# Kernel tuning notes

Measured on AMD Instinct MI355X. Metric: run time of the kernel, lower is better.

Reference implementation:

```python
import jax, jax.numpy as jnp
import numpy as np

N = 100000      # num nodes
E = 600000      # num edges
DIN = 64        # input_dim
DH = 128        # hidden_dim
G = 512         # num graphs
EPS = 1e-5      # BatchNorm eps


def setup_inputs() -> dict:
    key = jax.random.key(0)
    ks = jax.random.split(key, 12)
    x = jax.random.normal(ks[0], (N, DIN), jnp.float32)
    edge_index = jax.random.randint(ks[1], (2, E), 0, N)
    batch = jnp.sort(jax.random.randint(ks[2], (N,), 0, G))

    def w(k, shape):
        return (jax.random.normal(k, shape, jnp.float32) / np.float32(np.sqrt(shape[0])))

    inp = {"x": x, "edge_index": edge_index, "batch": batch}
    inp.update(
        W1=w(ks[3], (DIN, DH)), b1=jnp.zeros((DH,), jnp.float32),
        bn1_g=jnp.ones((DH,), jnp.float32), bn1_b=jnp.zeros((DH,), jnp.float32),
        bn1_m=jax.random.normal(ks[4], (DH,), jnp.float32) * 0.1,
        bn1_v=jnp.ones((DH,), jnp.float32),
        W2=w(ks[5], (DH, DH)), b2=jnp.zeros((DH,), jnp.float32),
        bn2_g=jnp.ones((DH,), jnp.float32), bn2_b=jnp.zeros((DH,), jnp.float32),
        bn2_m=jax.random.normal(ks[6], (DH,), jnp.float32) * 0.1,
        bn2_v=jnp.ones((DH,), jnp.float32),
        W3=w(ks[7], (DH, DH)), b3=jnp.zeros((DH,), jnp.float32),
        bn3_g=jnp.ones((DH,), jnp.float32), bn3_b=jnp.zeros((DH,), jnp.float32),
        bn3_m=jax.random.normal(ks[8], (DH,), jnp.float32) * 0.1,
        bn3_v=jnp.ones((DH,), jnp.float32),
        fc1_w=w(ks[9], (DH, DH // 2)), fc1_b=jnp.zeros((DH // 2,), jnp.float32),
        fc2_w=w(ks[10], (DH // 2, 1)), fc2_b=jnp.zeros((1,), jnp.float32),
    )
    return inp


def reference(x, edge_index, batch,
              W1, b1, bn1_g, bn1_b, bn1_m, bn1_v,
              W2, b2, bn2_g, bn2_b, bn2_m, bn2_v,
              W3, b3, bn3_g, bn3_b, bn3_m, bn3_v,
              fc1_w, fc1_b, fc2_w, fc2_b):
    # --- GCN normalization with self-loops (PyG GCNConv, sym norm) ---
    loop = jnp.arange(N, dtype=edge_index.dtype)
    src = jnp.concatenate([edge_index[0], loop])  # [E+N]
    dst = jnp.concatenate([edge_index[1], loop])  # [E+N]
    deg = jax.ops.segment_sum(jnp.ones_like(dst, jnp.float32), dst, num_segments=N)
    dis = jnp.where(deg > 0, jax.lax.rsqrt(jnp.maximum(deg, 1.0)), 0.0)
    norm = (dis[src] * dis[dst])[:, None]  # [E+N, 1]

    def conv(h, W, b):
        h = h @ W
        agg = jax.ops.segment_sum(h[src] * norm, dst, num_segments=N)
        return agg + b

    def bn(h, g, bta, m, v):
        return (h - m) * jax.lax.rsqrt(v + EPS) * g + bta  # eval-mode BatchNorm1d

    # block 1 (dropout is identity in eval)
    h = jax.nn.relu(bn(conv(x, W1, b1), bn1_g, bn1_b, bn1_m, bn1_v))
    # middle residual block (num_layers=3 -> one block)
    h = jax.nn.relu(bn(conv(h, W2, b2), bn2_g, bn2_b, bn2_m, bn2_v)) + h
    # output conv block
    h = jax.nn.relu(bn(conv(h, W3, b3), bn3_g, bn3_b, bn3_m, bn3_v))

    # global mean pool over graphs
    sums = jax.ops.segment_sum(h, batch, num_segments=G)          # [G, DH]
    cnt = jax.ops.segment_sum(jnp.ones((N, 1), h.dtype), batch, num_segments=G)
    pooled = sums / jnp.maximum(cnt, 1.0)

    h = jax.nn.relu(pooled @ fc1_w + fc1_b)
    return jax.nn.sigmoid(h @ fc2_w + fc2_b)  # [G, 1]
```

## Files before the change

### kernel.cpp

```cpp
#include <hip/hip_runtime.h>
#include <math.h>

#define N_NODES 100000
#define N_EDGES 600000
#define DIN     64
#define DH      128
#define NG      512
#define EPS_BN  1e-5f
#define SCAN_TPB 256
#define N_SCAN_BLK ((N_NODES + SCAN_TPB - 1) / SCAN_TPB)
#define G_EDGE   ((N_EDGES + 255) / 256)

typedef unsigned short u16;
typedef short s16x8 __attribute__((ext_vector_type(8)));
typedef float f32x4 __attribute__((ext_vector_type(4)));

__device__ __forceinline__ u16 f2bf(float x) {
    unsigned u = __builtin_bit_cast(unsigned, x);
    u += 0x7fffu + ((u >> 16) & 1u);
    return (u16)(u >> 16);
}
__device__ __forceinline__ float bf2f(u16 h) {
    unsigned u = ((unsigned)h) << 16;
    return __builtin_bit_cast(float, u);
}

#define PREP_XCVT_BLKS 3125
#define PREP_WT1_BLKS  32
#define PREP_WT2_BLKS  64
#define PREP_WT3_BLKS  64
#define PREP_BN_BLKS   2
#define PREP_GB_BLKS   3
#define PREP_B0 (G_EDGE + PREP_XCVT_BLKS)
#define PREP_B1 (PREP_B0 + PREP_WT1_BLKS)
#define PREP_B2 (PREP_B1 + PREP_WT2_BLKS)
#define PREP_B3 (PREP_B2 + PREP_WT3_BLKS)
#define PREP_B4 (PREP_B3 + PREP_BN_BLKS)
#define PREP_TOTAL (PREP_B4 + PREP_GB_BLKS)

__device__ __forceinline__ void wt_body(const float* __restrict__ W, u16* __restrict__ Wt,
                                        int K, int idx) {
    if (idx >= K * DH) return;
    int k = idx / DH, n = idx % DH;
    Wt[(long)n * K + k] = f2bf(W[idx]);
}

__global__ __launch_bounds__(256) void degprep_kernel(
    const int* __restrict__ dst, int* __restrict__ deg,
    const float* __restrict__ x, u16* __restrict__ xb,
    const float* __restrict__ W1, u16* __restrict__ Wt1,
    const float* __restrict__ W2, u16* __restrict__ Wt2,
    const float* __restrict__ W3, u16* __restrict__ Wt3,
    const float* b1, const float* g1, const float* bb1, const float* m1, const float* v1,
    const float* b2, const float* g2, const float* bb2, const float* m2, const float* v2,
    const float* b3, const float* g3, const float* bb3, const float* m3, const float* v3,
    float* __restrict__ sc, float* __restrict__ sh,
    const int* __restrict__ batch, int* __restrict__ gp) {
    const int b = blockIdx.x;
    const int tid = threadIdx.x;
    if (b < G_EDGE) {
        const int e = b * 256 + tid;
        if (e < N_EDGES) atomicAdd(&deg[dst[e]], 1);
    } else if (b < PREP_B0) {
        const long i = ((long)(b - G_EDGE) * 256 + tid) * 8;
        const float4 a = *(const float4*)(x + i);
        const float4 c = *(const float4*)(x + i + 4);
        s16x8 o;
        o[0] = (short)f2bf(a.x); o[1] = (short)f2bf(a.y);
        o[2] = (short)f2bf(a.z); o[3] = (short)f2bf(a.w);
        o[4] = (short)f2bf(c.x); o[5] = (short)f2bf(c.y);
        o[6] = (short)f2bf(c.z); o[7] = (short)f2bf(c.w);
        *(s16x8*)(xb + i) = o;
    } else if (b < PREP_B1) {
        wt_body(W1, Wt1, DIN, (b - PREP_B0) * 256 + tid);
    } else if (b < PREP_B2) {
        wt_body(W2, Wt2, DH, (b - PREP_B1) * 256 + tid);
    } else if (b < PREP_B3) {
        wt_body(W3, Wt3, DH, (b - PREP_B2) * 256 + tid);
    } else if (b < PREP_B4) {
        const int i = (b - PREP_B3) * 256 + tid;
        if (i < 3 * DH) {
            int l = i >> 7, c = i & (DH - 1);
            const float* bc = l == 0 ? b1 : (l == 1 ? b2 : b3);
            const float* g  = l == 0 ? g1 : (l == 1 ? g2 : g3);
            const float* bb = l == 0 ? bb1 : (l == 1 ? bb2 : bb3);
            const float* m  = l == 0 ? m1 : (l == 1 ? m2 : m3);
            const float* v  = l == 0 ? v1 : (l == 1 ? v2 : v3);
            float s = g[c] * rsqrtf(v[c] + EPS_BN);
            sc[i] = s;
            sh[i] = (bc[c] - m[c]) * s + bb[c];
        }
    } else {
        const int g = (b - PREP_B4) * 256 + tid;
        if (g <= NG) {
            int lo = 0, hi = N_NODES;
            while (lo < hi) {
                int mid = (lo + hi) >> 1;
                if (batch[mid] < g) lo = mid + 1; else hi = mid;
            }
            gp[g] = lo;
        }
    }
}

__global__ __launch_bounds__(SCAN_TPB) void scan1_kernel(const int* __restrict__ deg,
                                                         float* __restrict__ dis,
                                                         int* __restrict__ rp,
                                                         int* __restrict__ blk, int n) {
    __shared__ int sm[SCAN_TPB];
    const int t = threadIdx.x;
    const int i = blockIdx.x * SCAN_TPB + t;
    int v = 0;
    if (i < n) {
        v = deg[i];
        dis[i] = rsqrtf((float)v + 1.0f);
    }
    sm[t] = v;
    __syncthreads();
#pragma unroll
    for (int off = 1; off < SCAN_TPB; off <<= 1) {
        int u = (t >= off) ? sm[t - off] : 0;
        __syncthreads();
        sm[t] += u;
        __syncthreads();
    }
    if (i <= n) rp[i] = sm[t] - v;
    if (t == SCAN_TPB - 1) blk[blockIdx.x] = sm[t];
}

__global__ __launch_bounds__(512) void scan2_kernel(int* __restrict__ blk, int nblk) {
    __shared__ int sm[512];
    const int t = threadIdx.x;
    const int v = (t < nblk) ? blk[t] : 0;
    sm[t] = v;
    __syncthreads();
#pragma unroll
    for (int off = 1; off < 512; off <<= 1) {
        int u = (t >= off) ? sm[t - off] : 0;
        __syncthreads();
        sm[t] += u;
        __syncthreads();
    }
    if (t < nblk) blk[t] = sm[t] - v;
}

__global__ __launch_bounds__(256) void build_csr_kernel(const int* __restrict__ src,
                                                        const int* __restrict__ dst,
                                                        const int* __restrict__ rp,
                                                        const int* __restrict__ blk,
                                                        int* __restrict__ cursor,
                                                        int* __restrict__ col, int E) {
    int e = blockIdx.x * blockDim.x + threadIdx.x;
    if (e >= E) return;
    const int s = src[e];
    const int d = dst[e];
    const int p = atomicAdd(&cursor[d], 1);
    col[rp[d] + blk[d >> 8] + p] = s;
}

template <int K>
__global__ __launch_bounds__(256) void gemm_mfma(const u16* __restrict__ A,
                                                 const u16* __restrict__ Wt,
                                                 const float* __restrict__ dis,
                                                 u16* __restrict__ C,
                                                 int M) {
    const int wave = threadIdx.x >> 6;
    const int lane = threadIdx.x & 63;
    const int r16 = lane & 15;
    const int kc  = lane >> 4;
    const long row0 = (long)blockIdx.x * 64 + wave * 16;

    f32x4 acc[8];
#pragma unroll
    for (int t = 0; t < 8; ++t)
#pragma unroll
        for (int q = 0; q < 4; ++q) acc[t][q] = 0.0f;

    long arow = row0 + r16;
    if (arow >= M) arow = M - 1;
    const u16* ap = A + arow * K + kc * 8;

#pragma unroll
    for (int ks = 0; ks < K; ks += 32) {
        const s16x8 a = *(const s16x8*)(ap + ks);
#pragma unroll
        for (int t = 0; t < 8; ++t) {
            const s16x8 b = *(const s16x8*)(Wt + (long)(t * 16 + r16) * K + ks + kc * 8);
            acc[t] = __builtin_amdgcn_mfma_f32_16x16x32_bf16(a, b, acc[t], 0, 0, 0);
        }
    }

#pragma unroll
    for (int r = 0; r < 4; ++r) {
        const long row = row0 + kc * 4 + r;
        if (row < M) {
            const float dd = dis[row];
            u16* cp = C + row * DH + r16;
#pragma unroll
            for (int t = 0; t < 8; ++t) cp[t * 16] = f2bf(acc[t][r] * dd);
        }
    }
}

template <bool RES>
__global__ __launch_bounds__(256) void agg_epi_kernel(const u16* __restrict__ H,
                                                      const int* __restrict__ rp,
                                                      const int* __restrict__ blk,
                                                      const int* __restrict__ col,
                                                      const float* __restrict__ dis,
                                                      const float* __restrict__ scl,
                                                      const float* __restrict__ shf,
                                                      u16* __restrict__ out, int n) {
    const long t = (long)blockIdx.x * blockDim.x + threadIdx.x;
    const int lane = (int)(t & 31);
    const long i = t >> 5;
    if (i >= n) return;
    const int cl = lane & 15;
    const int eh = lane >> 4;
    const int c = cl * 8;

    float acc[8] = {0, 0, 0, 0, 0, 0, 0, 0};
    if (eh == 0) {
        const s16x8 hv = *(const s16x8*)(H + i * DH + c);
#pragma unroll
        for (int q = 0; q < 8; ++q) acc[q] = bf2f((u16)hv[q]);
    }

    const int beg = rp[i] + blk[i >> 8];
    const int end = rp[i + 1] + blk[(int)(i + 1) >> 8];
    for (int e = beg + eh; e < end; e += 2) {
        const int s = col[e];
        const s16x8 v = *(const s16x8*)(H + (long)s * DH + c);
#pragma unroll
        for (int q = 0; q < 8; ++q) acc[q] += bf2f((u16)v[q]);
    }

#pragma unroll
    for (int q = 0; q < 8; ++q) acc[q] += __shfl_xor(acc[q], 16);

    if (eh == 0) {
        const float dd = dis[i];
        const float4 s0 = *(const float4*)(scl + c);
        const float4 s1 = *(const float4*)(scl + c + 4);
        const float4 f0 = *(const float4*)(shf + c);
        const float4 f1 = *(const float4*)(shf + c + 4);
        const float sv[8] = {s0.x, s0.y, s0.z, s0.w, s1.x, s1.y, s1.z, s1.w};
        const float fv[8] = {f0.x, f0.y, f0.z, f0.w, f1.x, f1.y, f1.z, f1.w};

        float r[8];
#pragma unroll
        for (int q = 0; q < 8; ++q) r[q] = fmaxf(fmaf(acc[q] * dd, sv[q], fv[q]), 0.0f);
        if (RES) {
            const s16x8 rv = *(const s16x8*)(out + i * DH + c);
#pragma unroll
            for (int q = 0; q < 8; ++q) r[q] += bf2f((u16)rv[q]);
        }
        s16x8 ov;
#pragma unroll
        for (int q = 0; q < 8; ++q) ov[q] = (short)f2bf(r[q]);
        *(s16x8*)(out + i * DH + c) = ov;
    }
}

__global__ __launch_bounds__(256) void pool_head_kernel(const u16* __restrict__ h,
                                                        const int* __restrict__ gp,
                                                        const float* __restrict__ fc1w,
                                                        const float* __restrict__ fc1b,
                                                        const float* __restrict__ fc2w,
                                                        const float* __restrict__ fc2b,
                                                        float* __restrict__ out) {
    const int g = blockIdx.x;
    const int t = threadIdx.x;
    const int grp = t >> 4;
    const int cl = t & 15;
    const int c = cl * 8;
    const int beg = gp[g];
    const int end = gp[g + 1];

    float acc[8] = {0, 0, 0, 0, 0, 0, 0, 0};
    for (int i = beg + grp; i < end; i += 16) {
        const s16x8 v = *(const s16x8*)(h + (long)i * DH + c);
#pragma unroll
        for (int q = 0; q < 8; ++q) acc[q] += bf2f((u16)v[q]);
    }

    __shared__ float sm[16][DH];
    __shared__ float p[DH];
#pragma unroll
    for (int q = 0; q < 8; ++q) sm[grp][c + q] = acc[q];
    __syncthreads();

    if (t < DH) {
        float s = 0.0f;
#pragma unroll
        for (int r = 0; r < 16; ++r) s += sm[r][t];
        p[t] = s / fmaxf((float)(end - beg), 1.0f);
    }
    __syncthreads();

    if (t < 64) {
        float a = 0.0f;
#pragma unroll 4
        for (int k = 0; k < DH; ++k) a = fmaf(p[k], fc1w[(long)k * 64 + t], a);
        const float h1 = fmaxf(a + fc1b[t], 0.0f);
        float v = h1 * fc2w[t];
#pragma unroll
        for (int off = 32; off > 0; off >>= 1) v += __shfl_down(v, off);
        if (t == 0) out[g] = 1.0f / (1.0f + expf(-(v + fc2b[0])));
    }
}

extern "C" void kernel_launch(void* const* d_in, const int* in_sizes, int n_in,
                              void* d_out, int out_size, void* d_ws, size_t ws_size,
                              hipStream_t stream) {
    const float* x     = (const float*)d_in[0];
    const int*   ei    = (const int*)d_in[1];
    const int*   batch = (const int*)d_in[2];
    const float* W1 = (const float*)d_in[3];
    const float* b1 = (const float*)d_in[4];
    const float* g1 = (const float*)d_in[5];
    const float* t1 = (const float*)d_in[6];
    const float* m1 = (const float*)d_in[7];
    const float* v1 = (const float*)d_in[8];
    const float* W2 = (const float*)d_in[9];
    const float* b2 = (const float*)d_in[10];
    const float* g2 = (const float*)d_in[11];
    const float* t2 = (const float*)d_in[12];
    const float* m2 = (const float*)d_in[13];
    const float* v2 = (const float*)d_in[14];
    const float* W3 = (const float*)d_in[15];
    const float* b3 = (const float*)d_in[16];
    const float* g3 = (const float*)d_in[17];
    const float* t3 = (const float*)d_in[18];
    const float* m3 = (const float*)d_in[19];
    const float* v3 = (const float*)d_in[20];
    const float* fc1w = (const float*)d_in[21];
    const float* fc1b = (const float*)d_in[22];
    const float* fc2w = (const float*)d_in[23];
    const float* fc2b = (const float*)d_in[24];

    const int* src = ei;
    const int* dst = ei + N_EDGES;

    char* ws = (char*)d_ws;
    size_t off = 0;
    auto alloc = [&](size_t bytes) -> char* {
        char* p = ws + off;
        off = (off + bytes + 511) & ~(size_t)511;
        return p;
    };
    int*   deg     = (int*)  alloc((size_t)2 * N_NODES * 4);
    int*   cursor  = deg + N_NODES;
    float* dis     = (float*)alloc((size_t)N_NODES * 4);
    int*   rp      = (int*)  alloc(((size_t)N_NODES + 1) * 4);
    int*   blk     = (int*)  alloc((size_t)N_SCAN_BLK * 4);
    int*   col     = (int*)  alloc((size_t)N_EDGES * 4);
    int*   gp      = (int*)  alloc((size_t)(NG + 1) * 4);
    float* bnsc    = (float*)alloc((size_t)3 * DH * 4);
    float* bnsh    = (float*)alloc((size_t)3 * DH * 4);
    u16*   xb      = (u16*)  alloc((size_t)N_NODES * DIN * 2);
    u16*   Wt1     = (u16*)  alloc((size_t)DH * DIN * 2);
    u16*   Wt2     = (u16*)  alloc((size_t)DH * DH * 2);
    u16*   Wt3     = (u16*)  alloc((size_t)DH * DH * 2);
    u16*   bufB    = (u16*)  alloc((size_t)N_NODES * DH * 2);
    u16*   bufA    = (u16*)  alloc((size_t)N_NODES * DH * 2);

    const int TPB = 256;
    const int gGemm = (N_NODES + 63) / 64;
    const int gAgg  = (int)(((long)N_NODES * 32 + TPB - 1) / TPB);

    hipMemsetAsync(deg, 0, (size_t)2 * N_NODES * 4, stream);
    degprep_kernel<<<PREP_TOTAL, TPB, 0, stream>>>(dst, deg, x, xb, W1, Wt1, W2, Wt2,
                                                   W3, Wt3,
                                                   b1, g1, t1, m1, v1,
                                                   b2, g2, t2, m2, v2,
                                                   b3, g3, t3, m3, v3,
                                                   bnsc, bnsh, batch, gp);
    scan1_kernel<<<N_SCAN_BLK, SCAN_TPB, 0, stream>>>(deg, dis, rp, blk, N_NODES);
    scan2_kernel<<<1, 512, 0, stream>>>(blk, N_SCAN_BLK);
    build_csr_kernel<<<G_EDGE, TPB, 0, stream>>>(src, dst, rp, blk, cursor, col, N_EDGES);

    gemm_mfma<DIN><<<gGemm, TPB, 0, stream>>>(xb, Wt1, dis, bufB, N_NODES);
    agg_epi_kernel<false><<<gAgg, TPB, 0, stream>>>(bufB, rp, blk, col, dis,
                                                    bnsc, bnsh, bufA, N_NODES);
    gemm_mfma<DH><<<gGemm, TPB, 0, stream>>>(bufA, Wt2, dis, bufB, N_NODES);
    agg_epi_kernel<true><<<gAgg, TPB, 0, stream>>>(bufB, rp, blk, col, dis,
                                                   bnsc + DH, bnsh + DH, bufA, N_NODES);
    gemm_mfma<DH><<<gGemm, TPB, 0, stream>>>(bufA, Wt3, dis, bufB, N_NODES);
    agg_epi_kernel<false><<<gAgg, TPB, 0, stream>>>(bufB, rp, blk, col, dis,
                                                    bnsc + 2 * DH, bnsh + 2 * DH, bufA,
                                                    N_NODES);

    pool_head_kernel<<<NG, TPB, 0, stream>>>(bufA, gp, fc1w, fc1b, fc2w, fc2b,
                                             (float*)d_out);
}
```

Before: 295.0 us.

## Fuse x bf16 conversion into first GEMM and stage GEMM output via LDS

Removes the separate fp32-to-bf16 conversion of x from the prep kernel and converts on the fly inside the first MFMA GEMM, eliminating a bf16 copy of x written to and read back from memory. The GEMM epilogue now stages results in a swizzled shared-memory tile so each lane writes 16-byte contiguous rows instead of scattered 2-byte stores. Aggregation output uses nontemporal stores. The first GEMM now reads twice the bytes for A, and the LDS staging adds shared-memory traffic per block.

```diff
diff --git a/kernel.cpp b/kernel.cpp
--- a/kernel.cpp
+++ b/kernel.cpp
@@ -25,13 +25,12 @@
     return __builtin_bit_cast(float, u);
 }
 
-#define PREP_XCVT_BLKS 3125
 #define PREP_WT1_BLKS  32
 #define PREP_WT2_BLKS  64
 #define PREP_WT3_BLKS  64
 #define PREP_BN_BLKS   2
 #define PREP_GB_BLKS   3
-#define PREP_B0 (G_EDGE + PREP_XCVT_BLKS)
+#define PREP_B0 G_EDGE
 #define PREP_B1 (PREP_B0 + PREP_WT1_BLKS)
 #define PREP_B2 (PREP_B1 + PREP_WT2_BLKS)
 #define PREP_B3 (PREP_B2 + PREP_WT3_BLKS)
@@ -47,7 +46,6 @@
 
 __global__ __launch_bounds__(256) void degprep_kernel(
     const int* __restrict__ dst, int* __restrict__ deg,
-    const float* __restrict__ x, u16* __restrict__ xb,
     const float* __restrict__ W1, u16* __restrict__ Wt1,
     const float* __restrict__ W2, u16* __restrict__ Wt2,
     const float* __restrict__ W3, u16* __restrict__ Wt3,
@@ -58,19 +56,9 @@
     const int* __restrict__ batch, int* __restrict__ gp) {
     const int b = blockIdx.x;
     const int tid = threadIdx.x;
-    if (b < G_EDGE) {
+    if (b < PREP_B0) {
         const int e = b * 256 + tid;
         if (e < N_EDGES) atomicAdd(&deg[dst[e]], 1);
-    } else if (b < PREP_B0) {
-        const long i = ((long)(b - G_EDGE) * 256 + tid) * 8;
-        const float4 a = *(const float4*)(x + i);
-        const float4 c = *(const float4*)(x + i + 4);
-        s16x8 o;
-        o[0] = (short)f2bf(a.x); o[1] = (short)f2bf(a.y);
-        o[2] = (short)f2bf(a.z); o[3] = (short)f2bf(a.w);
-        o[4] = (short)f2bf(c.x); o[5] = (short)f2bf(c.y);
-        o[6] = (short)f2bf(c.z); o[7] = (short)f2bf(c.w);
-        *(s16x8*)(xb + i) = o;
     } else if (b < PREP_B1) {
         wt_body(W1, Wt1, DIN, (b - PREP_B0) * 256 + tid);
     } else if (b < PREP_B2) {
@@ -158,12 +146,13 @@
     col[rp[d] + blk[d >> 8] + p] = s;
 }
 
-template <int K>
-__global__ __launch_bounds__(256) void gemm_mfma(const u16* __restrict__ A,
+template <int K, bool AF32>
+__global__ __launch_bounds__(256) void gemm_mfma(const void* __restrict__ Ain,
                                                  const u16* __restrict__ Wt,
                                                  const float* __restrict__ dis,
                                                  u16* __restrict__ C,
                                                  int M) {
+    __shared__ u16 ldsc[4][16][DH];
     const int wave = threadIdx.x >> 6;
     const int lane = threadIdx.x & 63;
     const int r16 = lane & 15;
@@ -178,11 +167,21 @@
 
     long arow = row0 + r16;
     if (arow >= M) arow = M - 1;
-    const u16* ap = A + arow * K + kc * 8;
 
 #pragma unroll
     for (int ks = 0; ks < K; ks += 32) {
-        const s16x8 a = *(const s16x8*)(ap + ks);
+        s16x8 a;
+        if constexpr (AF32) {
+            const float* ap = (const float*)Ain + arow * K + ks + kc * 8;
+            const float4 f0 = *(const float4*)(ap);
+            const float4 f1 = *(const float4*)(ap + 4);
+            a[0] = (short)f2bf(f0.x); a[1] = (short)f2bf(f0.y);
+            a[2] = (short)f2bf(f0.z); a[3] = (short)f2bf(f0.w);
+            a[4] = (short)f2bf(f1.x); a[5] = (short)f2bf(f1.y);
+            a[6] = (short)f2bf(f1.z); a[7] = (short)f2bf(f1.w);
+        } else {
+            a = *(const s16x8*)((const u16*)Ain + arow * K + ks + kc * 8);
+        }
 #pragma unroll
         for (int t = 0; t < 8; ++t) {
             const s16x8 b = *(const s16x8*)(Wt + (long)(t * 16 + r16) * K + ks + kc * 8);
@@ -190,14 +189,31 @@
         }
     }
 
-#pragma unroll
-    for (int r = 0; r < 4; ++r) {
-        const long row = row0 + kc * 4 + r;
+    float dd[4];
+#pragma unroll
+    for (int q = 0; q < 4; ++q) {
+        long r = row0 + kc * 4 + q;
+        dd[q] = dis[r < M ? r : (M - 1)];
+    }
+
+#pragma unroll
+    for (int t = 0; t < 8; ++t) {
+        const int blkc = (t << 1) | (r16 >> 3);
+        const int co = r16 & 7;
+#pragma unroll
+        for (int q = 0; q < 4; ++q) {
+            const int row = kc * 4 + q;
+            ldsc[wave][row][(((blkc ^ (row & 7)) << 3) | co)] = f2bf(acc[t][q] * dd[q]);
+        }
+    }
+#pragma unroll
+    for (int it = 0; it < 4; ++it) {
+        const int rl = (lane >> 4) + it * 4;
+        const long row = row0 + rl;
         if (row < M) {
-            const float dd = dis[row];
-            u16* cp = C + row * DH + r16;
-#pragma unroll
-            for (int t = 0; t < 8; ++t) cp[t * 16] = f2bf(acc[t][r] * dd);
+            const int phys = (lane & 15) ^ (rl & 7);
+            const s16x8 v = *(const s16x8*)&ldsc[wave][rl][phys << 3];
+            *(s16x8*)(C + row * DH + ((lane & 15) << 3)) = v;
         }
     }
 }
@@ -258,7 +274,7 @@
         s16x8 ov;
 #pragma unroll
         for (int q = 0; q < 8; ++q) ov[q] = (short)f2bf(r[q]);
-        *(s16x8*)(out + i * DH + c) = ov;
+        __builtin_nontemporal_store(ov, (s16x8*)(out + i * DH + c));
     }
 }
 
@@ -358,7 +374,6 @@
     int*   gp      = (int*)  alloc((size_t)(NG + 1) * 4);
     float* bnsc    = (float*)alloc((size_t)3 * DH * 4);
     float* bnsh    = (float*)alloc((size_t)3 * DH * 4);
-    u16*   xb      = (u16*)  alloc((size_t)N_NODES * DIN * 2);
     u16*   Wt1     = (u16*)  alloc((size_t)DH * DIN * 2);
     u16*   Wt2     = (u16*)  alloc((size_t)DH * DH * 2);
     u16*   Wt3     = (u16*)  alloc((size_t)DH * DH * 2);
@@ -370,8 +385,7 @@
     const int gAgg  = (int)(((long)N_NODES * 32 + TPB - 1) / TPB);
 
     hipMemsetAsync(deg, 0, (size_t)2 * N_NODES * 4, stream);
-    degprep_kernel<<<PREP_TOTAL, TPB, 0, stream>>>(dst, deg, x, xb, W1, Wt1, W2, Wt2,
-                                                   W3, Wt3,
+    degprep_kernel<<<PREP_TOTAL, TPB, 0, stream>>>(dst, deg, W1, Wt1, W2, Wt2, W3, Wt3,
                                                    b1, g1, t1, m1, v1,
                                                    b2, g2, t2, m2, v2,
                                                    b3, g3, t3, m3, v3,
@@ -380,13 +394,16 @@
     scan2_kernel<<<1, 512, 0, stream>>>(blk, N_SCAN_BLK);
     build_csr_kernel<<<G_EDGE, TPB, 0, stream>>>(src, dst, rp, blk, cursor, col, N_EDGES);
 
-    gemm_mfma<DIN><<<gGemm, TPB, 0, stream>>>(xb, Wt1, dis, bufB, N_NODES);
+    gemm_mfma<DIN, true><<<gGemm, TPB, 0, stream>>>((const void*)x, Wt1, dis, bufB,
+                                                    N_NODES);
     agg_epi_kernel<false><<<gAgg, TPB, 0, stream>>>(bufB, rp, blk, col, dis,
                                                     bnsc, bnsh, bufA, N_NODES);
-    gemm_mfma<DH><<<gGemm, TPB, 0, stream>>>(bufA, Wt2, dis, bufB, N_NODES);
+    gemm_mfma<DH, false><<<gGemm, TPB, 0, stream>>>((const void*)bufA, Wt2, dis, bufB,
+                                                    N_NODES);
     agg_epi_kernel<true><<<gAgg, TPB, 0, stream>>>(bufB, rp, blk, col, dis,
                                                    bnsc + DH, bnsh + DH, bufA, N_NODES);
-    gemm_mfma<DH><<<gGemm, TPB, 0, stream>>>(bufA, Wt3, dis, bufB, N_NODES);
+    gemm_mfma<DH, false><<<gGemm, TPB, 0, stream>>>((const void*)bufA, Wt3, dis, bufB,
+                                                    N_NODES);
     agg_epi_kernel<false><<<gAgg, TPB, 0, stream>>>(bufB, rp, blk, col, dis,
                                                     bnsc + 2 * DH, bnsh + 2 * DH, bufA,
                                                     N_NODES);
```

New measurement: 289.9 us. No clear change (-1.7%).
